# Performance work log

Measured on AMD Instinct MI355X. Metric: run time of the kernel, lower is better.

## Reference

```python
import jax, jax.numpy as jnp
import numpy as np

DEPTH, DIM, HEADS, DIM_HEAD, NBF, MULT = 2, 512, 8, 64, 256, 4
INNER = HEADS * DIM_HEAD


def layernorm(x, g, b, eps=1e-5):
    mu = jnp.mean(x, axis=-1, keepdims=True)
    var = jnp.mean((x - mu) ** 2, axis=-1, keepdims=True)
    return (x - mu) * jax.lax.rsqrt(var + eps) * g + b


def softmax_kernel(data, proj, is_query, eps=1e-4):
    # data: [b,h,n,d], proj: [m,d]  -> phi: [b,h,n,m]  (FAVOR+ positive features)
    d = data.shape[-1]
    normalizer = d ** -0.25
    ratio = proj.shape[0] ** -0.5
    data_dash = jnp.einsum('bhnd,md->bhnm', data * normalizer, proj)
    diag = jnp.sum(data ** 2, axis=-1, keepdims=True) * 0.5 * (normalizer ** 2)
    if is_query:
        m = jnp.max(data_dash, axis=-1, keepdims=True)
    else:
        m = jnp.max(data_dash, axis=(-2, -1), keepdims=True)
    m = jax.lax.stop_gradient(m)
    return ratio * (jnp.exp(data_dash - diag - m) + eps)


def setup_inputs() -> dict:
    key = jax.random.key(0)
    ks = jax.random.split(key, 16)
    s = 0.02
    B, N = 4, 8192
    inp = {
        'x': jax.random.normal(ks[0], (B, N, DIM), jnp.float32),
        'ln1_g': jnp.ones((DEPTH, DIM), jnp.float32),
        'ln1_b': jnp.zeros((DEPTH, DIM), jnp.float32),
        'ln2_g': jnp.ones((DEPTH, DIM), jnp.float32),
        'ln2_b': jnp.zeros((DEPTH, DIM), jnp.float32),
        'Wq': jax.random.normal(ks[1], (DEPTH, DIM, INNER), jnp.float32) * s,
        'bq': jnp.zeros((DEPTH, INNER), jnp.float32),
        'Wk': jax.random.normal(ks[2], (DEPTH, DIM, INNER), jnp.float32) * s,
        'bk': jnp.zeros((DEPTH, INNER), jnp.float32),
        'Wv': jax.random.normal(ks[3], (DEPTH, DIM, INNER), jnp.float32) * s,
        'bv': jnp.zeros((DEPTH, INNER), jnp.float32),
        'Wo': jax.random.normal(ks[4], (DEPTH, INNER, DIM), jnp.float32) * s,
        'bo': jnp.zeros((DEPTH, DIM), jnp.float32),
        'proj': jax.random.normal(ks[5], (DEPTH, NBF, DIM_HEAD), jnp.float32),
        'W1': jax.random.normal(ks[6], (DEPTH, DIM, DIM * MULT), jnp.float32) * s,
        'b1': jnp.zeros((DEPTH, DIM * MULT), jnp.float32),
        'W2': jax.random.normal(ks[7], (DEPTH, DIM * MULT, DIM), jnp.float32) * s,
        'b2': jnp.zeros((DEPTH, DIM), jnp.float32),
    }
    return inp


def reference(x, ln1_g, ln1_b, ln2_g, ln2_b, Wq, bq, Wk, bk, Wv, bv, Wo, bo, proj, W1, b1, W2, b2):
    B, N, D = x.shape
    for i in range(DEPTH):
        # --- PreLayerNorm + FAVOR+ self-attention, residual ---
        y = layernorm(x, ln1_g[i], ln1_b[i])
        q = (y @ Wq[i] + bq[i]).reshape(B, N, HEADS, DIM_HEAD).transpose(0, 2, 1, 3)
        k = (y @ Wk[i] + bk[i]).reshape(B, N, HEADS, DIM_HEAD).transpose(0, 2, 1, 3)
        v = (y @ Wv[i] + bv[i]).reshape(B, N, HEADS, DIM_HEAD).transpose(0, 2, 1, 3)
        qp = softmax_kernel(q, proj[i], True)   # [b,h,n,m]
        kp = softmax_kernel(k, proj[i], False)  # [b,h,n,m]
        # non-causal linear attention: O(n*m*d) instead of O(n^2)
        k_sum = kp.sum(axis=2)                               # [b,h,m]
        d_inv = 1.0 / jnp.einsum('bhnm,bhm->bhn', qp, k_sum)
        ctx = jnp.einsum('bhnm,bhnd->bhmd', kp, v)           # [b,h,m,d]
        o = jnp.einsum('bhmd,bhnm,bhn->bhnd', ctx, qp, d_inv)
        o = o.transpose(0, 2, 1, 3).reshape(B, N, INNER)
        x = x + o @ Wo[i] + bo[i]
        # --- PreLayerNorm + FeedForward (GELU), residual ---
        y = layernorm(x, ln2_g[i], ln2_b[i])
        h = jax.nn.gelu(y @ W1[i] + b1[i], approximate=False)
        x = x + h @ W2[i] + b2[i]
    return x
```

## Files before the change

kernel.cpp:

```cpp
#include <hip/hip_runtime.h>
#include <math.h>

#define DIMX 512
#define HEADS 8
#define DHEAD 64
#define NBFX 256
#define FFD 2048
#define NBX 4
#define SEQ 8192
#define TOK (NBX*SEQ)
#define NBH (NBX*HEADS)
#define VROWS 80
#define NCHUNK 8
#define BK 64

typedef unsigned short u16;
typedef __attribute__((ext_vector_type(8))) short short8;
typedef __attribute__((ext_vector_type(4))) float f32x4;

__device__ __forceinline__ float bf2f(u16 x){ return __uint_as_float(((unsigned)x)<<16); }
__device__ __forceinline__ u16 f2bf(float f){
  unsigned u=__float_as_uint(f);
  return (u16)((u + 0x7FFFu + ((u>>16)&1u))>>16);
}
__device__ __forceinline__ void gload16(const void* g, void* l){
  __builtin_amdgcn_global_load_lds((const __attribute__((address_space(1))) void*)g,
                                   (__attribute__((address_space(3))) void*)l, 16, 0, 0);
}
__device__ __forceinline__ float gelu_f(float v){
  float x=v*0.70710678118654752f;
  float ax=fabsf(x);
  float t=1.0f/(1.0f+0.3275911f*ax);
  float p=t*(0.254829592f+t*(-0.284496736f+t*(1.421413741f+t*(-1.453152027f+t*1.061405429f))));
  float erfv=1.0f-p*__expf(-ax*ax);
  erfv=(x<0.0f)? -erfv : erfv;
  return 0.5f*v*(1.0f+erfv);
}

#define FENCE asm volatile(""::: "memory")
#define BAR() do{ FENCE; __builtin_amdgcn_s_barrier(); FENCE; }while(0)

__global__ void copy_f32(const float4* __restrict__ s, float4* __restrict__ d, int n4){
  int i=blockIdx.x*blockDim.x+threadIdx.x;
  if(i<n4) d[i]=s[i];
}
__global__ void conv_x(const float* __restrict__ x, u16* __restrict__ t){
  int i=blockIdx.x*blockDim.x+threadIdx.x;
  const float* xr=x+(size_t)i*8;
  float4 a=*(const float4*)xr, b=*(const float4*)(xr+4);
  u16 pk[8]={f2bf(a.x),f2bf(a.y),f2bf(a.z),f2bf(a.w),f2bf(b.x),f2bf(b.y),f2bf(b.z),f2bf(b.w)};
  uint4 pv;
  pv.x=(unsigned)pk[0]|((unsigned)pk[1]<<16); pv.y=(unsigned)pk[2]|((unsigned)pk[3]<<16);
  pv.z=(unsigned)pk[4]|((unsigned)pk[5]<<16); pv.w=(unsigned)pk[6]|((unsigned)pk[7]<<16);
  *(uint4*)(t+(size_t)i*8)=pv;
}
__global__ void expand_k(const u16* __restrict__ t, float* __restrict__ o){
  int i=blockIdx.x*blockDim.x+threadIdx.x;
  short8 v=*(const short8*)(t+(size_t)i*8);
  float* orr=o+(size_t)i*8;
  float4 f0={bf2f((u16)v[0]),bf2f((u16)v[1]),bf2f((u16)v[2]),bf2f((u16)v[3])};
  float4 f1={bf2f((u16)v[4]),bf2f((u16)v[5]),bf2f((u16)v[6]),bf2f((u16)v[7])};
  *(float4*)orr=f0; *(float4*)(orr+4)=f1;
}
__global__ void conv_proj(const float* __restrict__ p, u16* __restrict__ o, int n){
  int i=blockIdx.x*blockDim.x+threadIdx.x;
  if(i<n) o[i]=f2bf(p[i]*0.35355339059327373f);
}
__global__ void convT(const float* __restrict__ src, u16* __restrict__ dst, int K, int Ncol){
  __shared__ float t[32][33];
  int k0=blockIdx.y*32, n0=blockIdx.x*32;
  int tx=threadIdx.x, ty=threadIdx.y;
  for(int i=ty;i<32;i+=8) t[i][tx]=src[(size_t)(k0+i)*Ncol + n0+tx];
  __syncthreads();
  for(int i=ty;i<32;i+=8) dst[(size_t)(n0+i)*K + k0+tx]=f2bf(t[tx][i]);
}
__global__ void fill_vt(u16* __restrict__ vt){
  int i=blockIdx.x*blockDim.x+threadIdx.x;
  int n=i&(SEQ-1); int r=(i>>13)&15; int bh=i>>17;
  vt[((size_t)bh*VROWS + 64 + r)*SEQ + n] = (r==0)? (u16)0x3F80 : (u16)0;
}
__global__ void pack_bias(const float* __restrict__ bq, const float* __restrict__ bk,
                          const float* __restrict__ bv, float* __restrict__ o){
  int i=blockIdx.x*blockDim.x+threadIdx.x;
  int l=i/1536, c=i-l*1536;
  const float* s=(c<512)? bq : ((c<1024)? bk : bv);
  o[i]=s[l*512 + (c&511)];
}

__global__ __launch_bounds__(256) void ln_k(const u16* __restrict__ x, const float* __restrict__ g,
                                            const float* __restrict__ b, u16* __restrict__ y){
  const int row=blockIdx.x*4 + (threadIdx.x>>6);
  const int ln=threadIdx.x&63;
  const u16* xr=x+(size_t)row*DIMX;
  short8 xv=*(const short8*)(xr+ln*8);
  float v[8];
  #pragma unroll
  for(int e=0;e<8;e++) v[e]=bf2f((u16)xv[e]);
  float s=0;
  #pragma unroll
  for(int e=0;e<8;e++) s+=v[e];
  #pragma unroll
  for(int m=1;m<64;m<<=1) s+=__shfl_xor(s,m);
  const float mean=s*(1.0f/DIMX);
  float s2=0;
  #pragma unroll
  for(int e=0;e<8;e++){ v[e]-=mean; s2+=v[e]*v[e]; }
  #pragma unroll
  for(int m=1;m<64;m<<=1) s2+=__shfl_xor(s2,m);
  const float rs=rsqrtf(s2*(1.0f/DIMX)+1e-5f);
  u16* yr=y+(size_t)row*DIMX+ln*8;
  u16 pk[8];
  #pragma unroll
  for(int e=0;e<8;e++) pk[e]=f2bf(v[e]*rs*g[ln*8+e]+b[ln*8+e]);
  uint4 pv;
  pv.x=(unsigned)pk[0]|((unsigned)pk[1]<<16); pv.y=(unsigned)pk[2]|((unsigned)pk[3]<<16);
  pv.z=(unsigned)pk[4]|((unsigned)pk[5]<<16); pv.w=(unsigned)pk[6]|((unsigned)pk[7]<<16);
  *(uint4*)yr=pv;
}

#define MFMA16(MH,BF,NH) do{                                                             \
  __builtin_amdgcn_s_setprio(1);                                                         \
  _Pragma("unroll") for(int kk_=0;kk_<2;kk_++)                                           \
    _Pragma("unroll") for(int i_=0;i_<4;i_++)                                            \
      _Pragma("unroll") for(int j_=0;j_<2;j_++)                                          \
        acc[MH][i_][NH][j_]=__builtin_amdgcn_mfma_f32_16x16x32_bf16(af[i_][kk_],BF[j_][kk_],acc[MH][i_][NH][j_],0,0,0); \
  __builtin_amdgcn_s_setprio(0);                                                         \
}while(0)

#define STG(T,HALF,ISB,BUF) do{ if((T)<nt){                                              \
  gload16(gp[ISB][HALF][0]+(size_t)(T)*BK, &lds[BUF][ISB][(HALF)*128 +    wv*8][0]);     \
  gload16(gp[ISB][HALF][1]+(size_t)(T)*BK, &lds[BUF][ISB][(HALF)*128 + 64+wv*8][0]); } }while(0)

#define LDA(BUF,MH) do{                                                                  \
  _Pragma("unroll") for(int i_=0;i_<4;i_++)                                              \
    _Pragma("unroll") for(int kk_=0;kk_<2;kk_++)                                         \
      af[i_][kk_]=*(const short8*)((const u16*)lds[BUF][0] + aoffs[MH][i_][kk_]); }while(0)

#define LDB(BF,BUF,NH) do{                                                               \
  _Pragma("unroll") for(int j_=0;j_<2;j_++)                                              \
    _Pragma("unroll") for(int kk_=0;kk_<2;kk_++)                                         \
      BF[j_][kk_]=*(const short8*)((const u16*)lds[BUF][1] + boffs[NH][j_][kk_]); }while(0)

#define TILE(T,BUF,OBUF) do{                                                             \
  LDB(bf0,BUF,0); LDA(BUF,0);                                                            \
  STG((T)+1,1,0,OBUF);                                                                   \
  BAR(); MFMA16(0,bf0,0); BAR();                                                         \
  LDB(bf1,BUF,1);                                                                        \
  STG((T)+1,1,1,OBUF);                                                                   \
  BAR(); MFMA16(0,bf1,1); BAR();                                                         \
  LDA(BUF,1);                                                                            \
  STG((T)+2,0,1,BUF);                                                                    \
  BAR(); MFMA16(1,bf0,0); BAR();                                                         \
  STG((T)+2,0,0,BUF);                                                                    \
  BAR(); MFMA16(1,bf1,1);                                                                \
  if((T)+2<nt) asm volatile("s_waitcnt vmcnt(4)":::"memory");                            \
  else         asm volatile("s_waitcnt vmcnt(0)":::"memory");                            \
  BAR();                                                                                 \
}while(0)

template<int EPI,int K>
__global__ __launch_bounds__(512,2) void gemm256(const u16* __restrict__ A, const u16* __restrict__ Bt,
                                                 const float* __restrict__ bias, void* __restrict__ outp,
                                                 u16* __restrict__ out2, int Ncol){
  constexpr int nt=K/BK;
  constexpr int HS=(K==2048)?1:2;
  constexpr int H=1<<HS;
  __shared__ u16 lds[2][2][256][64];
  const int tid=threadIdx.x, wv=tid>>6, ln=tid&63;
  const int wr=wv>>2, wc=wv&3;
  const int gx=gridDim.x;
  const int P=blockIdx.y*gx+blockIdx.x;
  const int grp=8*H*gx;
  const int G=P/grp, R=P-G*grp;
  const int xcd=R&7, s=R>>3;
  const int by=(G*8+xcd)*H + (s&(H-1));
  const int bx=s>>HS;
  const int m0=by*256, n0=bx*256;
  f32x4 acc[2][4][2][2]={};

  const u16* gp[2][2][2];
  #pragma unroll
  for(int isB=0;isB<2;isB++)
    #pragma unroll
    for(int half=0;half<2;half++)
      #pragma unroll
      for(int ss=0;ss<2;ss++){
        int Gg=ss*512+wv*64+ln;
        int arow=half*128+(Gg>>3), g=Gg&7;
        const u16* src=isB? Bt:A;
        int b0=isB? n0:m0;
        gp[isB][half][ss]=src+(size_t)(b0+arow)*K+((g^(arow&7))<<3);
      }
  int aoffs[2][4][2], boffs[2][2][2];
  #pragma unroll
  for(int mh=0;mh<2;mh++)
    #pragma unroll
    for(int i=0;i<4;i++){
      int row=wr*128+mh*64+i*16+(ln&15);
      #pragma unroll
      for(int kk=0;kk<2;kk++)
        aoffs[mh][i][kk]=row*64+((((kk*4+(ln>>4)))^(row&7))<<3);
    }
  #pragma unroll
  for(int nh=0;nh<2;nh++)
    #pragma unroll
    for(int j=0;j<2;j++){
      int row=wc*64+nh*32+j*16+(ln&15);
      #pragma unroll
      for(int kk=0;kk<2;kk++)
        boffs[nh][j][kk]=row*64+((((kk*4+(ln>>4)))^(row&7))<<3);
    }

  short8 af[4][2], bf0[2][2], bf1[2][2];

  STG(0,0,0,0); STG(0,1,0,0); STG(0,0,1,0); STG(0,1,1,0);
  STG(1,0,1,1); STG(1,0,0,1);
  asm volatile("s_waitcnt vmcnt(4)":::"memory");
  BAR();

  #pragma unroll 1
  for(int t=0;t<nt;t+=2){
    TILE(t,0,1);
    TILE(t+1,1,0);
  }

  #pragma unroll
  for(int mh=0;mh<2;mh++)
  #pragma unroll
  for(int i=0;i<4;i++)
  #pragma unroll
  for(int nh=0;nh<2;nh++)
  #pragma unroll
  for(int j=0;j<2;j++){
    const int row=m0+wr*128+mh*64+i*16+(ln>>4)*4;
    const int col=n0+wc*64+nh*32+j*16+(ln&15);
    const float bv=bias[col];
    const f32x4 a=acc[mh][i][nh][j];
    if constexpr(EPI==0){
      if(col<1024){
        u16* o=(u16*)outp + (size_t)(col>>9)*TOK*DIMX + (col&511);
        #pragma unroll
        for(int r=0;r<4;r++) o[(size_t)(row+r)*DIMX]=f2bf(a[r]+bv);
      } else {
        const int hd=col-1024, h_=hd>>6, d_=hd&63, b_=row>>13, nn=row&(SEQ-1);
        u16 pk[4];
        #pragma unroll
        for(int r=0;r<4;r++) pk[r]=f2bf(a[r]+bv);
        uint2 pv; pv.x=(unsigned)pk[0]|((unsigned)pk[1]<<16); pv.y=(unsigned)pk[2]|((unsigned)pk[3]<<16);
        *(uint2*)&out2[((size_t)(b_*HEADS+h_)*VROWS+d_)*SEQ+nn]=pv;
      }
    } else if constexpr(EPI==1){
      u16* o=(u16*)outp;
      #pragma unroll
      for(int r=0;r<4;r++){
        size_t ix=(size_t)(row+r)*Ncol+col;
        o[ix]=f2bf(bf2f(o[ix])+a[r]+bv);
      }
    } else {
      u16* o=(u16*)outp;
      #pragma unroll
      for(int r=0;r<4;r++)
        o[(size_t)(row+r)*Ncol+col]=f2bf(gelu_f(a[r]+bv));
    }
  }
}

__global__ __launch_bounds__(256) void vsum_k(const u16* __restrict__ vt, float* __restrict__ vs){
  const int gw=blockIdx.x*4 + (threadIdx.x>>6);
  const int ln=threadIdx.x&63;
  const int bh=gw/65, d=gw-bh*65;
  const u16* row=vt+((size_t)bh*VROWS+d)*SEQ;
  float s=0;
  for(int it=0;it<16;it++){
    short8 v=*(const short8*)&row[it*512+ln*8];
    #pragma unroll
    for(int e=0;e<8;e++) s+=bf2f((u16)v[e]);
  }
  #pragma unroll
  for(int m=1;m<64;m<<=1) s+=__shfl_xor(s,m);
  if(ln==0) vs[bh*80+d]=s;
}

__global__ __launch_bounds__(256) void kctx(const u16* __restrict__ kb, const u16* __restrict__ pj,
                                            const u16* __restrict__ vt,
                                            float* __restrict__ part, float* __restrict__ maxb){
  __shared__ u16 kl[64*64];
  __shared__ u16 vl[80*64];
  __shared__ u16 kp_l[128*64];
  __shared__ float dgl[64];
  const int kc=blockIdx.x, half=blockIdx.y, bh=blockIdx.z, b_=bh>>3, h_=bh&7;
  const int tid=threadIdx.x, wv=tid>>6, ln=tid&63;
  short8 pjf[2][2];
  #pragma unroll
  for(int i=0;i<2;i++)
    #pragma unroll
    for(int t=0;t<2;t++)
      pjf[i][t]=*(const short8*)&pj[(size_t)(half*128+wv*32+i*16+(ln&15))*DHEAD + t*32 + (ln>>4)*8];
  f32x4 ctx[2][5]={};
  float m_run=-3.0e38f;
  const u16* vbh=vt+(size_t)bh*VROWS*SEQ;
  for(int s=0;s<16;s++){
    const int n0s=kc*1024+s*64;
    const u16* kg=kb+((size_t)(b_*SEQ+n0s))*DIMX + h_*DHEAD;
    #pragma unroll
    for(int cc=0;cc<2;cc++){
      int c=cc*256+wv*64+ln; int t=c>>3, g=c&7;
      gload16(kg+(size_t)t*DIMX+((g^(t&7))*8), &kl[(size_t)(cc*256+wv*64)*8]);
    }
    #pragma unroll
    for(int cc=0;cc<2;cc++){
      int c=cc*256+wv*64+ln; int d=c>>3, g=c&7;
      gload16(vbh+(size_t)d*SEQ+n0s+((g^(d&7))*8), &vl[(size_t)(cc*256+wv*64)*8]);
    }
    if(wv<2){
      int c=512+wv*64+ln; int d=c>>3, g=c&7;
      gload16(vbh+(size_t)d*SEQ+n0s+((g^(d&7))*8), &vl[(size_t)(512+wv*64)*8]);
    }
    __syncthreads();
    if(tid<64){
      float ss=0;
      #pragma unroll
      for(int gg=0;gg<8;gg++){
        short8 kv=*(const short8*)&kl[tid*64 + ((gg+tid)&7)*8];
        #pragma unroll
        for(int e=0;e<8;e++){ float x=bf2f((u16)kv[e]); ss+=x*x; }
      }
      dgl[tid]=ss*0.0625f;
    }
    __syncthreads();
    f32x4 dd[2][4]={};
    #pragma unroll
    for(int tk=0;tk<2;tk++)
      #pragma unroll
      for(int j=0;j<4;j++){
        short8 bk_=*(const short8*)&kl[(j*16+(ln&15))*64 + (((tk*4+(ln>>4))^(ln&7))<<3)];
        #pragma unroll
        for(int i=0;i<2;i++)
          dd[i][j]=__builtin_amdgcn_mfma_f32_16x16x32_bf16(pjf[i][tk],bk_,dd[i][j],0,0,0);
      }
    float mt=-3.0e38f;
    #pragma unroll
    for(int i=0;i<2;i++)
      #pragma unroll
      for(int j=0;j<4;j++)
        #pragma unroll
        for(int r=0;r<4;r++) mt=fmaxf(mt,dd[i][j][r]);
    #pragma unroll
    for(int m=1;m<64;m<<=1) mt=fmaxf(mt,__shfl_xor(mt,m));
    if(mt>m_run){
      float sc=__expf(m_run-mt);
      #pragma unroll
      for(int i=0;i<2;i++)
        #pragma unroll
        for(int j2=0;j2<5;j2++) ctx[i][j2]*=sc;
      m_run=mt;
    }
    #pragma unroll
    for(int j=0;j<4;j++){
      const float dgn=dgl[j*16+(ln&15)];
      #pragma unroll
      for(int i=0;i<2;i++)
        #pragma unroll
        for(int r=0;r<4;r++){
          int m_l=wv*32+i*16+(ln>>4)*4+r;
          float E=__expf(dd[i][j][r]-dgn-m_run);
          kp_l[m_l*64 + (((j*2+((ln>>3)&1))^(m_l&7))<<3) + (ln&7)]=f2bf(E);
        }
    }
    #pragma unroll
    for(int tk=0;tk<2;tk++){
      short8 af2[2];
      #pragma unroll
      for(int i=0;i<2;i++)
        af2[i]=*(const short8*)&kp_l[(wv*32+i*16+(ln&15))*64 + (((tk*4+(ln>>4))^(ln&7))<<3)];
      #pragma unroll
      for(int j2=0;j2<5;j2++){
        short8 bf2=*(const short8*)&vl[(j2*16+(ln&15))*64 + (((tk*4+(ln>>4))^(ln&7))<<3)];
        #pragma unroll
        for(int i=0;i<2;i++)
          ctx[i][j2]=__builtin_amdgcn_mfma_f32_16x16x32_bf16(af2[i],bf2,ctx[i][j2],0,0,0);
      }
    }
    __syncthreads();
  }
  float* po=part + ((size_t)(bh*NCHUNK+kc))*(256*80) + (size_t)half*128*80;
  #pragma unroll
  for(int i=0;i<2;i++)
    #pragma unroll
    for(int j2=0;j2<5;j2++)
      #pragma unroll
      for(int r=0;r<4;r++)
        po[(size_t)(wv*32+i*16+(ln>>4)*4+r)*80 + j2*16+(ln&15)]=ctx[i][j2][r];
  if(ln==0) maxb[bh*64 + kc*8 + half*4 + wv]=m_run;
}

__global__ __launch_bounds__(256) void ctx_reduce(const float* __restrict__ part, const float* __restrict__ maxb,
                                                  const float* __restrict__ vs,
                                                  u16* __restrict__ ctxT, float* __restrict__ ksum){
  __shared__ float mx_s[64];
  __shared__ float sc_s[NCHUNK];
  const int mseg=blockIdx.x, bh=blockIdx.y, tid=threadIdx.x;
  if(tid<64) mx_s[tid]=maxb[(size_t)bh*64+tid];
  __syncthreads();
  float km=-3.0e38f;
  for(int i=0;i<64;i++) km=fmaxf(km,mx_s[i]);
  const int m0=mseg*32;
  const int half=m0>>7, wvv=(m0&127)>>5;
  if(tid<NCHUNK) sc_s[tid]=__expf(mx_s[tid*8+half*4+wvv]-km);
  __syncthreads();
  for(int rep=0;rep<10;rep++){
    int idx=rep*256+tid;
    int mo=idx/80, d=idx-mo*80;
    int m=m0+mo;
    float s=0;
    #pragma unroll
    for(int c=0;c<NCHUNK;c++)
      s+=sc_s[c]*part[((size_t)(bh*NCHUNK+c))*(256*80) + (size_t)m*80 + d];
    float vsd=(d<=64)? vs[bh*80+d] : 0.0f;
    float val=0.0625f*(s + 1e-4f*vsd);
    if(d<64)       ctxT[((size_t)bh*64+d)*NBFX + m]=f2bf(val);
    else if(d==64) ksum[bh*NBFX+m]=val;
  }
}

__global__ void csum_k(const u16* __restrict__ ctxT, const float* __restrict__ ksum, float* __restrict__ cs){
  const int bh=blockIdx.x, t=threadIdx.x;
  if(t<64){
    const u16* r=ctxT+((size_t)bh*64+t)*NBFX;
    float s=0;
    for(int m=0;m<NBFX;m+=8){
      short8 v=*(const short8*)&r[m];
      #pragma unroll
      for(int e=0;e<8;e++) s+=bf2f((u16)v[e]);
    }
    cs[bh*80+t]=s;
  } else if(t==64){
    float s=0;
    for(int m=0;m<NBFX;m++) s+=ksum[bh*NBFX+m];
    cs[bh*80+64]=s;
  }
}

__global__ __launch_bounds__(256) void q_fused(const u16* __restrict__ qb, const u16* __restrict__ pj,
                                               const u16* __restrict__ ctxT, const float* __restrict__ ksum,
                                               const float* __restrict__ cs, u16* __restrict__ ob){
  __shared__ u16 ql[64*64];
  __shared__ u16 qpl[64*136];
  __shared__ float dgs[64];
  __shared__ float mred[4*64], dred[4*64];
  __shared__ float ff_s[64], dinv_s[64];
  const int bh=blockIdx.y, b_=bh>>3, h_=bh&7;
  const int n0=blockIdx.x*64;
  const int tid=threadIdx.x, wv=tid>>6, ln=tid&63;
  const u16* qg=qb+((size_t)(b_*SEQ+n0))*DIMX + h_*DHEAD;
  #pragma unroll
  for(int cc=0;cc<2;cc++){
    int c=cc*256+wv*64+ln; int t=c>>3, g=c&7;
    gload16(qg+(size_t)t*DIMX+((g^(t&7))*8), &ql[(size_t)(cc*256+wv*64)*8]);
  }
  short8 pjf[2][2][2];
  float ks[2][2][4];
  #pragma unroll
  for(int h=0;h<2;h++)
    #pragma unroll
    for(int i=0;i<2;i++){
      #pragma unroll
      for(int t=0;t<2;t++)
        pjf[h][i][t]=*(const short8*)&pj[(size_t)(h*128+wv*32+i*16+(ln&15))*DHEAD + t*32 + (ln>>4)*8];
      #pragma unroll
      for(int r=0;r<4;r++)
        ks[h][i][r]=ksum[bh*NBFX + h*128+wv*32+i*16+(ln>>4)*4+r];
    }
  const float KS=cs[bh*80+64];
  __syncthreads();
  if(tid<64){
    float ss=0;
    #pragma unroll
    for(int gg=0;gg<8;gg++){
      short8 kv=*(const short8*)&ql[tid*64 + ((gg+tid)&7)*8];
      #pragma unroll
      for(int e=0;e<8;e++){ float x=bf2f((u16)kv[e]); ss+=x*x; }
    }
    dgs[tid]=ss*0.0625f;
  }
  __syncthreads();
  float mxp[4]={-3.0e38f,-3.0e38f,-3.0e38f,-3.0e38f};
  float dnp[4]={0,0,0,0};
  f32x4 oc[4]={};
  const u16* cb=ctxT+(size_t)bh*64*NBFX;
  #pragma unroll
  for(int h=0;h<2;h++){
    #pragma unroll
    for(int j=0;j<4;j++){
      f32x4 dq[2]={};
      #pragma unroll
      for(int tk=0;tk<2;tk++){
        short8 bq=*(const short8*)&ql[(j*16+(ln&15))*64 + (((tk*4+(ln>>4))^(ln&7))<<3)];
        #pragma unroll
        for(int i=0;i<2;i++)
          dq[i]=__builtin_amdgcn_mfma_f32_16x16x32_bf16(pjf[h][i][tk],bq,dq[i],0,0,0);
      }
      const float dgn=dgs[j*16+(ln&15)];
      #pragma unroll
      for(int i=0;i<2;i++)
        #pragma unroll
        for(int r=0;r<4;r++){
          float d_=dq[i][r];
          mxp[j]=fmaxf(mxp[j],d_);
          float E=__expf(d_-dgn);
          dnp[j]+=E*ks[h][i][r];
          qpl[(j*16+(ln&15))*136 + wv*32+i*16+(ln>>4)*4+r]=f2bf(E);
        }
    }
    __syncthreads();
    #pragma unroll
    for(int mk2=0;mk2<4;mk2++){
      short8 aq=*(const short8*)&cb[(size_t)(wv*16+(ln&15))*NBFX + h*128 + mk2*32 + (ln>>4)*8];
      #pragma unroll
      for(int j2=0;j2<4;j2++){
        short8 bqp=*(const short8*)&qpl[(j2*16+(ln&15))*136 + mk2*32 + (ln>>4)*8];
        oc[j2]=__builtin_amdgcn_mfma_f32_16x16x32_bf16(aq,bqp,oc[j2],0,0,0);
      }
    }
    __syncthreads();
  }
  #pragma unroll
  for(int j=0;j<4;j++){
    #pragma unroll
    for(int msk=16;msk<64;msk<<=1){
      mxp[j]=fmaxf(mxp[j],__shfl_xor(mxp[j],msk));
      dnp[j]+=__shfl_xor(dnp[j],msk);
    }
  }
  if(ln<16){
    #pragma unroll
    for(int j=0;j<4;j++){ mred[wv*64+j*16+ln]=mxp[j]; dred[wv*64+j*16+ln]=dnp[j]; }
  }
  __syncthreads();
  if(tid<64){
    float mx=fmaxf(fmaxf(mred[tid],mred[64+tid]),fmaxf(mred[128+tid],mred[192+tid]));
    float dn=dred[tid]+dred[64+tid]+dred[128+tid]+dred[192+tid];
    float f=1e-4f*__expf(mx);
    ff_s[tid]=f;
    dinv_s[tid]=1.0f/(dn + f*KS);
  }
  __syncthreads();
  float csr[4];
  #pragma unroll
  for(int r=0;r<4;r++) csr[r]=cs[bh*80 + wv*16+(ln>>4)*4+r];
  u16* og=ob+((size_t)(b_*SEQ+n0))*DIMX + h_*DHEAD;
  #pragma unroll
  for(int j2=0;j2<4;j2++){
    int n=j2*16+(ln&15);
    float f=ff_s[n], di=dinv_s[n];
    u16 pk[4];
    #pragma unroll
    for(int r=0;r<4;r++) pk[r]=f2bf((oc[j2][r]+f*csr[r])*di);
    uint2 pv; pv.x=(unsigned)pk[0]|((unsigned)pk[1]<<16); pv.y=(unsigned)pk[2]|((unsigned)pk[3]<<16);
    *(uint2*)&og[(size_t)n*DIMX + wv*16+(ln>>4)*4]=pv;
  }
}

static constexpr size_t SZ_ACT=(size_t)TOK*DIMX*2;
static constexpr size_t O_X=0;
static constexpr size_t O_Y=SZ_ACT, O_Q=2*SZ_ACT, O_K=3*SZ_ACT;
static constexpr size_t O_VT=4*SZ_ACT;
static constexpr size_t SZ_VT=(size_t)NBH*VROWS*SEQ*2;
static constexpr size_t O_PART=O_VT+SZ_VT;
static constexpr size_t SZ_PART=(size_t)NBH*NCHUNK*256*80*4;
static constexpr size_t O_CTXT=O_PART+SZ_PART;
static constexpr size_t SZ_CTXT=(size_t)NBH*64*NBFX*2;
static constexpr size_t O_KSUM=O_CTXT+SZ_CTXT;
static constexpr size_t SZ_KSUM=(size_t)NBH*NBFX*4;
static constexpr size_t O_MAX=O_KSUM+SZ_KSUM;
static constexpr size_t SZ_MAX=(size_t)NBH*64*4;
static constexpr size_t O_VSUM=O_MAX+SZ_MAX;
static constexpr size_t SZ_VSUM=(size_t)NBH*80*4;
static constexpr size_t O_CS=O_VSUM+SZ_VSUM;
static constexpr size_t SZ_CS=(size_t)NBH*80*4;
static constexpr size_t O_WQKV=(size_t)192*1024*1024;
static_assert(O_CS+SZ_CS <= O_WQKV, "small buffers must end below weight region");
static constexpr size_t SZ_WQKV=(size_t)2*1536*DIMX*2;
static constexpr size_t O_WOT=O_WQKV+SZ_WQKV;
static constexpr size_t SZ_W=(size_t)2*DIMX*DIMX*2;
static constexpr size_t O_W1T=O_WOT+SZ_W;
static constexpr size_t SZ_W1=(size_t)2*FFD*DIMX*2;
static constexpr size_t O_W2T=O_W1T+SZ_W1;
static constexpr size_t O_PJ=O_W2T+SZ_W1;
static constexpr size_t O_QKVB=O_PJ+(size_t)2*NBFX*DHEAD*2;
static constexpr size_t WS_END=O_QKVB+(size_t)2*1536*4;

extern "C" void kernel_launch(void* const* d_in, const int* in_sizes, int n_in,
                              void* d_out, int out_size, void* d_ws, size_t ws_size,
                              hipStream_t stream){
  (void)in_sizes;(void)n_in;(void)out_size;
  const float* xin =(const float*)d_in[0];
  const float* ln1g=(const float*)d_in[1];
  const float* ln1b=(const float*)d_in[2];
  const float* ln2g=(const float*)d_in[3];
  const float* ln2b=(const float*)d_in[4];
  const float* Wq=(const float*)d_in[5];
  const float* bq=(const float*)d_in[6];
  const float* Wk=(const float*)d_in[7];
  const float* bk=(const float*)d_in[8];
  const float* Wv=(const float*)d_in[9];
  const float* bv=(const float*)d_in[10];
  const float* Wo=(const float*)d_in[11];
  const float* bo=(const float*)d_in[12];
  const float* proj=(const float*)d_in[13];
  const float* W1=(const float*)d_in[14];
  const float* b1=(const float*)d_in[15];
  const float* W2=(const float*)d_in[16];
  const float* b2=(const float*)d_in[17];
  float* xout=(float*)d_out;

  if(ws_size < WS_END){
    copy_f32<<<(TOK*DIMX/4)/256,256,0,stream>>>((const float4*)xin,(float4*)xout, TOK*DIMX/4);
    return;
  }

  char* ws=(char*)d_ws;
  u16* xtr  =(u16*)(ws+O_X);
  u16* ybuf =(u16*)(ws+O_Y);
  u16* qbuf =(u16*)(ws+O_Q);
  u16* kbuf =(u16*)(ws+O_K);
  u16* vtb  =(u16*)(ws+O_VT);
  float* partb=(float*)(ws+O_PART);
  u16* ctxtb=(u16*)(ws+O_CTXT);
  float* ksumb=(float*)(ws+O_KSUM);
  float* maxb=(float*)(ws+O_MAX);
  float* vsumb=(float*)(ws+O_VSUM);
  float* csb=(float*)(ws+O_CS);
  u16* wqkvt=(u16*)(ws+O_WQKV);
  u16* wot=(u16*)(ws+O_WOT);
  u16* w1t=(u16*)(ws+O_W1T); u16* w2t=(u16*)(ws+O_W2T);
  u16* pjb=(u16*)(ws+O_PJ);
  float* qkvb=(float*)(ws+O_QKVB);
  u16* hbuf=(u16*)(ws+O_Q);

  for(int l=0;l<2;l++){
    size_t wo=(size_t)l*DIMX*DIMX;
    convT<<<dim3(16,16),dim3(32,8),0,stream>>>(Wq+wo, wqkvt+(size_t)(l*1536+   0)*DIMX, DIMX, DIMX);
    convT<<<dim3(16,16),dim3(32,8),0,stream>>>(Wk+wo, wqkvt+(size_t)(l*1536+ 512)*DIMX, DIMX, DIMX);
    convT<<<dim3(16,16),dim3(32,8),0,stream>>>(Wv+wo, wqkvt+(size_t)(l*1536+1024)*DIMX, DIMX, DIMX);
    convT<<<dim3(16,16),dim3(32,8),0,stream>>>(Wo+wo, wot+wo, DIMX, DIMX);
    size_t w1o=(size_t)l*DIMX*FFD;
    convT<<<dim3(64,16),dim3(32,8),0,stream>>>(W1+w1o, w1t+w1o, DIMX, FFD);
    convT<<<dim3(16,64),dim3(32,8),0,stream>>>(W2+w1o, w2t+w1o, FFD, DIMX);
  }
  conv_proj<<<(2*NBFX*DHEAD)/256,256,0,stream>>>(proj, pjb, 2*NBFX*DHEAD);
  pack_bias<<<12,256,0,stream>>>(bq,bk,bv,qkvb);
  conv_x<<<(TOK*DIMX/8)/256,256,0,stream>>>(xin, xtr);

  for(int l=0;l<2;l++){
    const u16* wqkvt_l=wqkvt+(size_t)l*1536*DIMX;
    const u16* wot_l=wot+(size_t)l*DIMX*DIMX;
    const u16* w1t_l=w1t+(size_t)l*DIMX*FFD;
    const u16* w2t_l=w2t+(size_t)l*DIMX*FFD;
    const u16* pj_l =pjb+(size_t)l*NBFX*DHEAD;
    const float* qkvb_l=qkvb+(size_t)l*1536;

    ln_k<<<TOK/4,256,0,stream>>>(xtr, ln1g+l*DIMX, ln1b+l*DIMX, ybuf);
    fill_vt<<<(NBH*16*SEQ)/256,256,0,stream>>>(vtb);
    gemm256<0,512><<<dim3(6,128),512,0,stream>>>(ybuf, wqkvt_l, qkvb_l, qbuf, vtb, 1536);
    vsum_k<<<520,256,0,stream>>>(vtb, vsumb);
    kctx<<<dim3(NCHUNK,2,32),256,0,stream>>>(kbuf, pj_l, vtb, partb, maxb);
    ctx_reduce<<<dim3(8,32),256,0,stream>>>(partb, maxb, vsumb, ctxtb, ksumb);
    csum_k<<<32,256,0,stream>>>(ctxtb, ksumb, csb);
    q_fused<<<dim3(128,32),256,0,stream>>>(qbuf, pj_l, ctxtb, ksumb, csb, ybuf);
    gemm256<1,512><<<dim3(2,128),512,0,stream>>>(ybuf, wot_l, bo+l*DIMX, xtr, nullptr, DIMX);
    ln_k<<<TOK/4,256,0,stream>>>(xtr, ln2g+l*DIMX, ln2b+l*DIMX, ybuf);
    gemm256<2,512><<<dim3(8,128),512,0,stream>>>(ybuf, w1t_l, b1+l*FFD, hbuf, nullptr, FFD);
    gemm256<1,2048><<<dim3(2,128),512,0,stream>>>(hbuf, w2t_l, b2+l*DIMX, xtr, nullptr, DIMX);
  }
  expand_k<<<(TOK*DIMX/8)/256,256,0,stream>>>(xtr, xout);
}
```

Baseline: 1.004 ms.

## Fuse fp32 input/output conversion into layernorm and GEMM epilogues; merge kctx halves

Removes the standalone conv_x and expand_k passes. The first layernorm now reads the fp32 input directly, the first Wo GEMM adds the fp32 residual in its epilogue, and the final W2 GEMM writes the fp32 output from the bf16 residual. This saves two full-tensor memory passes and two launches. kctx also moves from two 256-thread blocks per chunk to one 512-thread block covering all 256 features, so the K and V tiles are loaded once rather than twice, at the cost of more shared memory per block and fewer blocks.

```diff
diff --git a/kernel.cpp b/kernel.cpp
--- a/kernel.cpp
+++ b/kernel.cpp
@@ -44,24 +44,6 @@
   int i=blockIdx.x*blockDim.x+threadIdx.x;
   if(i<n4) d[i]=s[i];
 }
-__global__ void conv_x(const float* __restrict__ x, u16* __restrict__ t){
-  int i=blockIdx.x*blockDim.x+threadIdx.x;
-  const float* xr=x+(size_t)i*8;
-  float4 a=*(const float4*)xr, b=*(const float4*)(xr+4);
-  u16 pk[8]={f2bf(a.x),f2bf(a.y),f2bf(a.z),f2bf(a.w),f2bf(b.x),f2bf(b.y),f2bf(b.z),f2bf(b.w)};
-  uint4 pv;
-  pv.x=(unsigned)pk[0]|((unsigned)pk[1]<<16); pv.y=(unsigned)pk[2]|((unsigned)pk[3]<<16);
-  pv.z=(unsigned)pk[4]|((unsigned)pk[5]<<16); pv.w=(unsigned)pk[6]|((unsigned)pk[7]<<16);
-  *(uint4*)(t+(size_t)i*8)=pv;
-}
-__global__ void expand_k(const u16* __restrict__ t, float* __restrict__ o){
-  int i=blockIdx.x*blockDim.x+threadIdx.x;
-  short8 v=*(const short8*)(t+(size_t)i*8);
-  float* orr=o+(size_t)i*8;
-  float4 f0={bf2f((u16)v[0]),bf2f((u16)v[1]),bf2f((u16)v[2]),bf2f((u16)v[3])};
-  float4 f1={bf2f((u16)v[4]),bf2f((u16)v[5]),bf2f((u16)v[6]),bf2f((u16)v[7])};
-  *(float4*)orr=f0; *(float4*)(orr+4)=f1;
-}
 __global__ void conv_proj(const float* __restrict__ p, u16* __restrict__ o, int n){
   int i=blockIdx.x*blockDim.x+threadIdx.x;
   if(i<n) o[i]=f2bf(p[i]*0.35355339059327373f);
@@ -96,6 +78,35 @@
   float v[8];
   #pragma unroll
   for(int e=0;e<8;e++) v[e]=bf2f((u16)xv[e]);
+  float s=0;
+  #pragma unroll
+  for(int e=0;e<8;e++) s+=v[e];
+  #pragma unroll
+  for(int m=1;m<64;m<<=1) s+=__shfl_xor(s,m);
+  const float mean=s*(1.0f/DIMX);
+  float s2=0;
+  #pragma unroll
+  for(int e=0;e<8;e++){ v[e]-=mean; s2+=v[e]*v[e]; }
+  #pragma unroll
+  for(int m=1;m<64;m<<=1) s2+=__shfl_xor(s2,m);
+  const float rs=rsqrtf(s2*(1.0f/DIMX)+1e-5f);
+  u16* yr=y+(size_t)row*DIMX+ln*8;
+  u16 pk[8];
+  #pragma unroll
+  for(int e=0;e<8;e++) pk[e]=f2bf(v[e]*rs*g[ln*8+e]+b[ln*8+e]);
+  uint4 pv;
+  pv.x=(unsigned)pk[0]|((unsigned)pk[1]<<16); pv.y=(unsigned)pk[2]|((unsigned)pk[3]<<16);
+  pv.z=(unsigned)pk[4]|((unsigned)pk[5]<<16); pv.w=(unsigned)pk[6]|((unsigned)pk[7]<<16);
+  *(uint4*)yr=pv;
+}
+__global__ __launch_bounds__(256) void ln_f32(const float* __restrict__ x, const float* __restrict__ g,
+                                              const float* __restrict__ b, u16* __restrict__ y){
+  const int row=blockIdx.x*4 + (threadIdx.x>>6);
+  const int ln=threadIdx.x&63;
+  const float* xr=x+(size_t)row*DIMX;
+  float4 v0=*(const float4*)&xr[ln*8];
+  float4 v1=*(const float4*)&xr[ln*8+4];
+  float v[8]={v0.x,v0.y,v0.z,v0.w,v1.x,v1.y,v1.z,v1.w};
   float s=0;
   #pragma unroll
   for(int e=0;e<8;e++) s+=v[e];
@@ -161,7 +172,8 @@
 template<int EPI,int K>
 __global__ __launch_bounds__(512,2) void gemm256(const u16* __restrict__ A, const u16* __restrict__ Bt,
                                                  const float* __restrict__ bias, void* __restrict__ outp,
-                                                 u16* __restrict__ out2, int Ncol){
+                                                 u16* __restrict__ out2, const void* __restrict__ aux,
+                                                 int Ncol){
   constexpr int nt=K/BK;
   constexpr int HS=(K==2048)?1:2;
   constexpr int H=1<<HS;
@@ -256,11 +268,27 @@
         size_t ix=(size_t)(row+r)*Ncol+col;
         o[ix]=f2bf(bf2f(o[ix])+a[r]+bv);
       }
-    } else {
+    } else if constexpr(EPI==2){
       u16* o=(u16*)outp;
       #pragma unroll
       for(int r=0;r<4;r++)
         o[(size_t)(row+r)*Ncol+col]=f2bf(gelu_f(a[r]+bv));
+    } else if constexpr(EPI==3){
+      u16* o=(u16*)outp;
+      const float* ax=(const float*)aux;
+      #pragma unroll
+      for(int r=0;r<4;r++){
+        size_t ix=(size_t)(row+r)*Ncol+col;
+        o[ix]=f2bf(ax[ix]+a[r]+bv);
+      }
+    } else {
+      float* o=(float*)outp;
+      const u16* ax=(const u16*)aux;
+      #pragma unroll
+      for(int r=0;r<4;r++){
+        size_t ix=(size_t)(row+r)*Ncol+col;
+        o[ix]=bf2f(ax[ix])+a[r]+bv;
+      }
     }
   }
 }
@@ -281,40 +309,38 @@
   if(ln==0) vs[bh*80+d]=s;
 }
 
-__global__ __launch_bounds__(256) void kctx(const u16* __restrict__ kb, const u16* __restrict__ pj,
+__global__ __launch_bounds__(512) void kctx(const u16* __restrict__ kb, const u16* __restrict__ pj,
                                             const u16* __restrict__ vt,
                                             float* __restrict__ part, float* __restrict__ maxb){
   __shared__ u16 kl[64*64];
   __shared__ u16 vl[80*64];
-  __shared__ u16 kp_l[128*64];
+  __shared__ u16 kp_l[256*64];
   __shared__ float dgl[64];
-  const int kc=blockIdx.x, half=blockIdx.y, bh=blockIdx.z, b_=bh>>3, h_=bh&7;
+  const int kc=blockIdx.x, bh=blockIdx.y, b_=bh>>3, h_=bh&7;
   const int tid=threadIdx.x, wv=tid>>6, ln=tid&63;
   short8 pjf[2][2];
   #pragma unroll
   for(int i=0;i<2;i++)
     #pragma unroll
     for(int t=0;t<2;t++)
-      pjf[i][t]=*(const short8*)&pj[(size_t)(half*128+wv*32+i*16+(ln&15))*DHEAD + t*32 + (ln>>4)*8];
+      pjf[i][t]=*(const short8*)&pj[(size_t)(wv*32+i*16+(ln&15))*DHEAD + t*32 + (ln>>4)*8];
   f32x4 ctx[2][5]={};
   float m_run=-3.0e38f;
   const u16* vbh=vt+(size_t)bh*VROWS*SEQ;
   for(int s=0;s<16;s++){
     const int n0s=kc*1024+s*64;
     const u16* kg=kb+((size_t)(b_*SEQ+n0s))*DIMX + h_*DHEAD;
-    #pragma unroll
-    for(int cc=0;cc<2;cc++){
-      int c=cc*256+wv*64+ln; int t=c>>3, g=c&7;
-      gload16(kg+(size_t)t*DIMX+((g^(t&7))*8), &kl[(size_t)(cc*256+wv*64)*8]);
-    }
-    #pragma unroll
-    for(int cc=0;cc<2;cc++){
-      int c=cc*256+wv*64+ln; int d=c>>3, g=c&7;
-      gload16(vbh+(size_t)d*SEQ+n0s+((g^(d&7))*8), &vl[(size_t)(cc*256+wv*64)*8]);
-    }
-    if(wv<2){
-      int c=512+wv*64+ln; int d=c>>3, g=c&7;
-      gload16(vbh+(size_t)d*SEQ+n0s+((g^(d&7))*8), &vl[(size_t)(512+wv*64)*8]);
+    {
+      int t=tid>>3, g=tid&7;
+      gload16(kg+(size_t)t*DIMX+((g^(t&7))*8), &kl[(size_t)tid*8]);
+    }
+    {
+      int d=tid>>3, g=tid&7;
+      gload16(vbh+(size_t)d*SEQ+n0s+((g^(d&7))*8), &vl[(size_t)tid*8]);
+    }
+    if(tid<128){
+      int c=512+tid; int d=c>>3, g=c&7;
+      gload16(vbh+(size_t)d*SEQ+n0s+((g^(d&7))*8), &vl[(size_t)c*8]);
     }
     __syncthreads();
     if(tid<64){
@@ -383,7 +409,7 @@
     }
     __syncthreads();
   }
-  float* po=part + ((size_t)(bh*NCHUNK+kc))*(256*80) + (size_t)half*128*80;
+  float* po=part + ((size_t)(bh*NCHUNK+kc))*(256*80);
   #pragma unroll
   for(int i=0;i<2;i++)
     #pragma unroll
@@ -391,7 +417,7 @@
       #pragma unroll
       for(int r=0;r<4;r++)
         po[(size_t)(wv*32+i*16+(ln>>4)*4+r)*80 + j2*16+(ln&15)]=ctx[i][j2][r];
-  if(ln==0) maxb[bh*64 + kc*8 + half*4 + wv]=m_run;
+  if(ln==0) maxb[bh*64 + kc*8 + wv]=m_run;
 }
 
 __global__ __launch_bounds__(256) void ctx_reduce(const float* __restrict__ part, const float* __restrict__ maxb,
@@ -405,8 +431,7 @@
   float km=-3.0e38f;
   for(int i=0;i<64;i++) km=fmaxf(km,mx_s[i]);
   const int m0=mseg*32;
-  const int half=m0>>7, wvv=(m0&127)>>5;
-  if(tid<NCHUNK) sc_s[tid]=__expf(mx_s[tid*8+half*4+wvv]-km);
+  if(tid<NCHUNK) sc_s[tid]=__expf(mx_s[tid*8+mseg]-km);
   __syncthreads();
   for(int rep=0;rep<10;rep++){
     int idx=rep*256+tid;
@@ -650,7 +675,6 @@
   }
   conv_proj<<<(2*NBFX*DHEAD)/256,256,0,stream>>>(proj, pjb, 2*NBFX*DHEAD);
   pack_bias<<<12,256,0,stream>>>(bq,bk,bv,qkvb);
-  conv_x<<<(TOK*DIMX/8)/256,256,0,stream>>>(xin, xtr);
 
   for(int l=0;l<2;l++){
     const u16* wqkvt_l=wqkvt+(size_t)l*1536*DIMX;
@@ -660,18 +684,20 @@
     const u16* pj_l =pjb+(size_t)l*NBFX*DHEAD;
     const float* qkvb_l=qkvb+(size_t)l*1536;
 
-    ln_k<<<TOK/4,256,0,stream>>>(xtr, ln1g+l*DIMX, ln1b+l*DIMX, ybuf);
+    if(l==0) ln_f32<<<TOK/4,256,0,stream>>>(xin, ln1g, ln1b, ybuf);
+    else     ln_k<<<TOK/4,256,0,stream>>>(xtr, ln1g+l*DIMX, ln1b+l*DIMX, ybuf);
     fill_vt<<<(NBH*16*SEQ)/256,256,0,stream>>>(vtb);
-    gemm256<0,512><<<dim3(6,128),512,0,stream>>>(ybuf, wqkvt_l, qkvb_l, qbuf, vtb, 1536);
+    gemm256<0,512><<<dim3(6,128),512,0,stream>>>(ybuf, wqkvt_l, qkvb_l, qbuf, vtb, nullptr, 1536);
     vsum_k<<<520,256,0,stream>>>(vtb, vsumb);
-    kctx<<<dim3(NCHUNK,2,32),256,0,stream>>>(kbuf, pj_l, vtb, partb, maxb);
+    kctx<<<dim3(NCHUNK,32),512,0,stream>>>(kbuf, pj_l, vtb, partb, maxb);
     ctx_reduce<<<dim3(8,32),256,0,stream>>>(partb, maxb, vsumb, ctxtb, ksumb);
     csum_k<<<32,256,0,stream>>>(ctxtb, ksumb, csb);
     q_fused<<<dim3(128,32),256,0,stream>>>(qbuf, pj_l, ctxtb, ksumb, csb, ybuf);
-    gemm256<1,512><<<dim3(2,128),512,0,stream>>>(ybuf, wot_l, bo+l*DIMX, xtr, nullptr, DIMX);
+    if(l==0) gemm256<3,512><<<dim3(2,128),512,0,stream>>>(ybuf, wot_l, bo, xtr, nullptr, xin, DIMX);
+    else     gemm256<1,512><<<dim3(2,128),512,0,stream>>>(ybuf, wot_l, bo+l*DIMX, xtr, nullptr, nullptr, DIMX);
     ln_k<<<TOK/4,256,0,stream>>>(xtr, ln2g+l*DIMX, ln2b+l*DIMX, ybuf);
-    gemm256<2,512><<<dim3(8,128),512,0,stream>>>(ybuf, w1t_l, b1+l*FFD, hbuf, nullptr, FFD);
-    gemm256<1,2048><<<dim3(2,128),512,0,stream>>>(hbuf, w2t_l, b2+l*DIMX, xtr, nullptr, DIMX);
-  }
-  expand_k<<<(TOK*DIMX/8)/256,256,0,stream>>>(xtr, xout);
-}
+    gemm256<2,512><<<dim3(8,128),512,0,stream>>>(ybuf, w1t_l, b1+l*FFD, hbuf, nullptr, nullptr, FFD);
+    if(l==0) gemm256<1,2048><<<dim3(2,128),512,0,stream>>>(hbuf, w2t_l, b2, xtr, nullptr, nullptr, DIMX);
+    else     gemm256<4,2048><<<dim3(2,128),512,0,stream>>>(hbuf, w2t_l, b2+l*DIMX, xout, nullptr, xtr, DIMX);
+  }
+}
```

After: 975.5 us, median of 3. -2.8%, faster.
